# Optimization experiments

Measured on AMD Instinct MI355X. Metric: run time of the kernel, lower is better.

The kernel has to match this reference:

```python
import jax, jax.numpy as jnp
from jax import lax
import numpy as np

N, W, H, C = 32, 64, 64, 256
D_STYLE = 256


def setup_inputs() -> dict:
    key = jax.random.key(0)
    k1, k2, k3, k4 = jax.random.split(key, 4)
    inputs = jax.random.normal(k1, (N, W, H, C), dtype=jnp.float32)
    style_coding = jax.random.normal(k2, (N, D_STYLE), dtype=jnp.float32)
    # he_normal-ish init scaling for the learned weights
    w_dense = jax.random.normal(k3, (D_STYLE, C), dtype=jnp.float32) * np.sqrt(2.0 / D_STYLE)
    w_conv = jax.random.normal(k4, (1, 1, C, C), dtype=jnp.float32) * np.sqrt(2.0 / C)
    return {"inputs": inputs, "style_coding": style_coding, "w_dense": w_dense, "w_conv": w_conv}


def reference(inputs, style_coding, w_dense, w_conv):
    # inputs: [N,W,H,C] (NHWC), style_coding: [N,D_style]
    c = inputs.shape[-1]
    scale = 1.0 / jnp.sqrt(jnp.float32(c))
    # Dense(fout_dim, use_bias=False, activation=LeakyReLU())  (keras default alpha=0.3)
    q = jax.nn.leaky_relu(style_coding @ w_dense, negative_slope=0.3)  # [N,C]
    # channel-wise attention: einsum('nwhc,nwhc->nc') with q broadcast over w,h
    ca_logits = jnp.einsum('nwhc,nc->nc', inputs, q) * scale           # [N,C]
    ca = jax.nn.softmax(ca_logits, axis=-1)[:, None, None, :]          # [N,1,1,C]
    # position-wise attention: einsum('nwhc,nwhc->nwh'), softmax over flattened W*H
    pa_logits = jnp.einsum('nwhc,nc->nwh', inputs, q) * scale          # [N,W,H]
    n, w, h = pa_logits.shape
    pa = jax.nn.softmax(pa_logits.reshape(n, w * h), axis=1).reshape(n, w, h, 1)
    x = inputs * ca * pa                                               # [N,W,H,C]
    # DarknetConv2D_BN_Leaky with no norm kwarg: 1x1 conv (no bias) + LeakyReLU(0.1)
    y = lax.conv_general_dilated(x, w_conv, window_strides=(1, 1), padding='SAME',
                                 dimension_numbers=('NHWC', 'HWIO', 'NHWC'))
    return jax.nn.leaky_relu(y, negative_slope=0.1)
```

## Files before the change

kernel.cpp:

```cpp
#include <hip/hip_runtime.h>
#include <hip/hip_bf16.h>


#define NBATCH 32
#define PIX 4096
#define CH 256
#define SCALE 0.0625f

typedef __attribute__((ext_vector_type(8))) short short8;
typedef __attribute__((ext_vector_type(4))) short short4v;
typedef __attribute__((ext_vector_type(4))) float floatx4;

__device__ __forceinline__ short f2bf(float x) {
    unsigned u = __builtin_bit_cast(unsigned, x);
    u += 0x7fffu + ((u >> 16) & 1u);
    return (short)(u >> 16);
}

__global__ __launch_bounds__(256) void style_kernel(
    const float* __restrict__ style, const float* __restrict__ wd,
    float* __restrict__ q, float* __restrict__ colsum)
{
    __shared__ float s[256];
    const int n = blockIdx.x, t = threadIdx.x;
    s[t] = style[n * 256 + t];
    __syncthreads();
    float acc = 0.f;
#pragma unroll 8
    for (int k = 0; k < 256; ++k) acc += s[k] * wd[k * 256 + t];
    q[n * 256 + t] = acc > 0.f ? acc : 0.3f * acc;
    colsum[n * 256 + t] = 0.f;
}

__global__ __launch_bounds__(256) void reduce_convert_kernel(
    const float* __restrict__ inp, const float* __restrict__ q,
    float* __restrict__ colsum, float* __restrict__ pa_logits,
    short* __restrict__ in_bf)
{
    __shared__ float sm[4][256];
    const int n = blockIdx.y;
    const int chunk = blockIdx.x;
    const int lane = threadIdx.x & 63, w = threadIdx.x >> 6;
    const float4 qv = *(const float4*)&q[n * 256 + lane * 4];
    float4 cs = make_float4(0.f, 0.f, 0.f, 0.f);
    const int pbase = chunk * 128 + w * 32;
    const float* base = inp + ((size_t)n * PIX + pbase) * CH;
    short* bfb = in_bf + ((size_t)n * PIX + pbase) * CH;
    for (int j = 0; j < 32; ++j) {
        float4 v = *(const float4*)&base[(size_t)j * CH + lane * 4];
        short4v s;
        s.x = f2bf(v.x); s.y = f2bf(v.y); s.z = f2bf(v.z); s.w = f2bf(v.w);
        *(short4v*)&bfb[(size_t)j * CH + lane * 4] = s;
        float d = v.x * qv.x + v.y * qv.y + v.z * qv.z + v.w * qv.w;
        cs.x += v.x; cs.y += v.y; cs.z += v.z; cs.w += v.w;
#pragma unroll
        for (int off = 32; off; off >>= 1) d += __shfl_xor(d, off);
        if (lane == 0) pa_logits[n * PIX + pbase + j] = d * SCALE;
    }
    *(float4*)&sm[w][lane * 4] = cs;
    __syncthreads();
    const int t = threadIdx.x;
    float tot = sm[0][t] + sm[1][t] + sm[2][t] + sm[3][t];
    atomicAdd(&colsum[n * 256 + t], tot);
}

__global__ __launch_bounds__(256) void softmax_kernel(
    const float* __restrict__ colsum, const float* __restrict__ q,
    const float* __restrict__ pa_logits,
    float* __restrict__ ca, float* __restrict__ pa)
{
    __shared__ float red[256];
    const int n = blockIdx.x, t = threadIdx.x;

    float lg = colsum[n * 256 + t] * q[n * 256 + t] * SCALE;
    red[t] = lg; __syncthreads();
    for (int s = 128; s > 0; s >>= 1) {
        if (t < s) red[t] = fmaxf(red[t], red[t + s]);
        __syncthreads();
    }
    float m = red[0]; __syncthreads();
    float e = expf(lg - m);
    red[t] = e; __syncthreads();
    for (int s = 128; s > 0; s >>= 1) {
        if (t < s) red[t] += red[t + s];
        __syncthreads();
    }
    ca[n * 256 + t] = e / red[0];
    __syncthreads();

    float lv[16];
    float lmax = -1e30f;
#pragma unroll
    for (int i = 0; i < 16; ++i) {
        lv[i] = pa_logits[n * PIX + t + 256 * i];
        lmax = fmaxf(lmax, lv[i]);
    }
    red[t] = lmax; __syncthreads();
    for (int s = 128; s > 0; s >>= 1) {
        if (t < s) red[t] = fmaxf(red[t], red[t + s]);
        __syncthreads();
    }
    float M = red[0]; __syncthreads();
    float ev[16], lsum = 0.f;
#pragma unroll
    for (int i = 0; i < 16; ++i) { ev[i] = expf(lv[i] - M); lsum += ev[i]; }
    red[t] = lsum; __syncthreads();
    for (int s = 128; s > 0; s >>= 1) {
        if (t < s) red[t] += red[t + s];
        __syncthreads();
    }
    float inv = 1.0f / red[0];
#pragma unroll
    for (int i = 0; i < 16; ++i) pa[n * PIX + t + 256 * i] = ev[i] * inv;
}

__global__ void fold_kernel(const float* __restrict__ wc,
                            const float* __restrict__ ca,
                            short* __restrict__ wn)
{
    __shared__ float tile[32][33];
    const int co0 = blockIdx.x * 32, n = blockIdx.y;
    const int tx = threadIdx.x, ty = threadIdx.y;
    short* wout = wn + (size_t)n * 65536;
    for (int cit = 0; cit < 8; ++cit) {
        const int ci0 = cit * 32;
        if (cit) __syncthreads();
#pragma unroll
        for (int r = 0; r < 4; ++r)
            tile[ty + r * 8][tx] = wc[(ci0 + ty + r * 8) * 256 + co0 + tx];
        __syncthreads();
        const float cav = ca[n * 256 + ci0 + tx];
#pragma unroll
        for (int r = 0; r < 4; ++r)
            wout[(co0 + ty + r * 8) * 256 + ci0 + tx] = f2bf(tile[tx][ty + r * 8] * cav);
    }
}

__global__ __launch_bounds__(256) void conv_mfma(
    const short* __restrict__ in_bf, const float* __restrict__ pa,
    const short* __restrict__ wn, float* __restrict__ out)
{
    __shared__ __attribute__((aligned(16))) short As[128][72];
    __shared__ __attribute__((aligned(16))) short Bs[128][72];

    const int n   = blockIdx.z;
    const int m0  = blockIdx.y * 128;
    const int co0 = blockIdx.x * 128;
    const int tid = threadIdx.x;
    const int lane = tid & 63, wid = tid >> 6;
    const int wm = wid & 1, wn_ = wid >> 1;
    const int l16 = lane & 15, quad = lane >> 4;

    floatx4 acc[4][4] = {};

    const short* Abase = in_bf + ((size_t)(n * PIX + m0)) * CH;
    const short* Bbase = wn + (size_t)n * 65536 + (size_t)co0 * CH;

    const int g = tid & 7, r0 = tid >> 3;

    for (int kb = 0; kb < 4; ++kb) {
        const int k0 = kb * 64;
        if (kb) __syncthreads();
#pragma unroll
        for (int i = 0; i < 4; ++i) {
            const int r = r0 + 32 * i;
            *(uint4*)&As[r][g * 8] = *(const uint4*)&Abase[(size_t)r * CH + k0 + g * 8];
            *(uint4*)&Bs[r][g * 8] = *(const uint4*)&Bbase[(size_t)r * CH + k0 + g * 8];
        }
        __syncthreads();
#pragma unroll
        for (int kk = 0; kk < 64; kk += 32) {
            short8 af[4], bfr[4];
#pragma unroll
            for (int mt = 0; mt < 4; ++mt)
                af[mt] = *(const short8*)&As[wm * 64 + mt * 16 + l16][kk + quad * 8];
#pragma unroll
            for (int nt = 0; nt < 4; ++nt)
                bfr[nt] = *(const short8*)&Bs[wn_ * 64 + nt * 16 + l16][kk + quad * 8];
#pragma unroll
            for (int mt = 0; mt < 4; ++mt)
#pragma unroll
                for (int nt = 0; nt < 4; ++nt)
                    acc[mt][nt] = __builtin_amdgcn_mfma_f32_16x16x32_bf16(
                        af[mt], bfr[nt], acc[mt][nt], 0, 0, 0);
        }
    }

#pragma unroll
    for (int mt = 0; mt < 4; ++mt) {
#pragma unroll
        for (int reg = 0; reg < 4; ++reg) {
            const int pix = m0 + wm * 64 + mt * 16 + quad * 4 + reg;
            const float pav = pa[n * PIX + pix];
            float* orow = out + ((size_t)(n * PIX + pix)) * CH + co0 + wn_ * 64;
#pragma unroll
            for (int nt = 0; nt < 4; ++nt) {
                float z = acc[mt][nt][reg] * pav;
                orow[nt * 16 + l16] = z > 0.f ? z : 0.1f * z;
            }
        }
    }
}

extern "C" void kernel_launch(void* const* d_in, const int* in_sizes, int n_in,
                              void* d_out, int out_size, void* d_ws, size_t ws_size,
                              hipStream_t stream) {
    const float* inputs = (const float*)d_in[0];
    const float* style  = (const float*)d_in[1];
    const float* wdense = (const float*)d_in[2];
    const float* wconv  = (const float*)d_in[3];
    float* out = (float*)d_out;

    char* ws = (char*)d_ws;
    float* q         = (float*)(ws + 0);
    float* colsum    = (float*)(ws + 32768);
    float* ca        = (float*)(ws + 65536);
    float* pa_logits = (float*)(ws + 98304);
    float* pa        = (float*)(ws + 622592);
    short* wn        = (short*)(ws + 1146880);
    short* in_bf     = (short*)(ws + 5341184);

    style_kernel<<<NBATCH, 256, 0, stream>>>(style, wdense, q, colsum);
    reduce_convert_kernel<<<dim3(32, NBATCH), 256, 0, stream>>>(
        inputs, q, colsum, pa_logits, in_bf);
    softmax_kernel<<<NBATCH, 256, 0, stream>>>(colsum, q, pa_logits, ca, pa);
    fold_kernel<<<dim3(8, NBATCH), dim3(32, 8), 0, stream>>>(wconv, ca, wn);
    conv_mfma<<<dim3(2, 32, NBATCH), 256, 0, stream>>>(in_bf, pa, wn, out);
}
```

Measured before the change: 318.0 us.

## Fuse softmaxes into neighbors and load GEMM tiles directly to LDS

Drops the separate position softmax by accumulating exp-sums with atomics during the reduction pass and normalizing in the conv epilogue. It also merges the channel softmax into the weight-fold kernel, removing one launch and the ca/pa round trips. The conv staging switches to global_load_lds direct-to-LDS copies with an unpadded tile, which may add LDS bank conflicts on fragment reads. Skipping max subtraction risks overflow if logits are large.

Measured after the change: 322.9 us. No clear change (+1.5%).

```diff
diff --git a/kernel.cpp b/kernel.cpp
--- a/kernel.cpp
+++ b/kernel.cpp
@@ -11,6 +11,9 @@
 typedef __attribute__((ext_vector_type(4))) short short4v;
 typedef __attribute__((ext_vector_type(4))) float floatx4;
 
+typedef __attribute__((address_space(3))) unsigned lds_u32;
+typedef const __attribute__((address_space(1))) unsigned gbl_u32;
+
 __device__ __forceinline__ short f2bf(float x) {
     unsigned u = __builtin_bit_cast(unsigned, x);
     u += 0x7fffu + ((u >> 16) & 1u);
@@ -19,7 +22,7 @@
 
 __global__ __launch_bounds__(256) void style_kernel(
     const float* __restrict__ style, const float* __restrict__ wd,
-    float* __restrict__ q, float* __restrict__ colsum)
+    float* __restrict__ q, float* __restrict__ colsum, float* __restrict__ Ssum)
 {
     __shared__ float s[256];
     const int n = blockIdx.x, t = threadIdx.x;
@@ -30,12 +33,13 @@
     for (int k = 0; k < 256; ++k) acc += s[k] * wd[k * 256 + t];
     q[n * 256 + t] = acc > 0.f ? acc : 0.3f * acc;
     colsum[n * 256 + t] = 0.f;
+    if (t == 0) Ssum[n] = 0.f;
 }
 
 __global__ __launch_bounds__(256) void reduce_convert_kernel(
     const float* __restrict__ inp, const float* __restrict__ q,
     float* __restrict__ colsum, float* __restrict__ pa_logits,
-    short* __restrict__ in_bf)
+    float* __restrict__ Ssum, short* __restrict__ in_bf)
 {
     __shared__ float sm[4][256];
     const int n = blockIdx.y;
@@ -46,6 +50,7 @@
     const int pbase = chunk * 128 + w * 32;
     const float* base = inp + ((size_t)n * PIX + pbase) * CH;
     short* bfb = in_bf + ((size_t)n * PIX + pbase) * CH;
+    float es = 0.f;
     for (int j = 0; j < 32; ++j) {
         float4 v = *(const float4*)&base[(size_t)j * CH + lane * 4];
         short4v s;
@@ -55,8 +60,13 @@
         cs.x += v.x; cs.y += v.y; cs.z += v.z; cs.w += v.w;
 #pragma unroll
         for (int off = 32; off; off >>= 1) d += __shfl_xor(d, off);
-        if (lane == 0) pa_logits[n * PIX + pbase + j] = d * SCALE;
-    }
+        if (lane == 0) {
+            const float lg = d * SCALE;
+            pa_logits[n * PIX + pbase + j] = lg;
+            es += __expf(lg);
+        }
+    }
+    if (lane == 0) atomicAdd(&Ssum[n], es);
     *(float4*)&sm[w][lane * 4] = cs;
     __syncthreads();
     const int t = threadIdx.x;
@@ -64,13 +74,14 @@
     atomicAdd(&colsum[n * 256 + t], tot);
 }
 
-__global__ __launch_bounds__(256) void softmax_kernel(
+__global__ __launch_bounds__(256) void ca_fold_kernel(
     const float* __restrict__ colsum, const float* __restrict__ q,
-    const float* __restrict__ pa_logits,
-    float* __restrict__ ca, float* __restrict__ pa)
+    const float* __restrict__ wc, short* __restrict__ wn)
 {
     __shared__ float red[256];
-    const int n = blockIdx.x, t = threadIdx.x;
+    __shared__ float cas[256];
+    __shared__ float tile[32][33];
+    const int n = blockIdx.y, t = threadIdx.x;
 
     float lg = colsum[n * 256 + t] * q[n * 256 + t] * SCALE;
     red[t] = lg; __syncthreads();
@@ -79,48 +90,17 @@
         __syncthreads();
     }
     float m = red[0]; __syncthreads();
-    float e = expf(lg - m);
+    float e = __expf(lg - m);
     red[t] = e; __syncthreads();
     for (int s = 128; s > 0; s >>= 1) {
         if (t < s) red[t] += red[t + s];
         __syncthreads();
     }
-    ca[n * 256 + t] = e / red[0];
+    cas[t] = e / red[0];
     __syncthreads();
 
-    float lv[16];
-    float lmax = -1e30f;
-#pragma unroll
-    for (int i = 0; i < 16; ++i) {
-        lv[i] = pa_logits[n * PIX + t + 256 * i];
-        lmax = fmaxf(lmax, lv[i]);
-    }
-    red[t] = lmax; __syncthreads();
-    for (int s = 128; s > 0; s >>= 1) {
-        if (t < s) red[t] = fmaxf(red[t], red[t + s]);
-        __syncthreads();
-    }
-    float M = red[0]; __syncthreads();
-    float ev[16], lsum = 0.f;
-#pragma unroll
-    for (int i = 0; i < 16; ++i) { ev[i] = expf(lv[i] - M); lsum += ev[i]; }
-    red[t] = lsum; __syncthreads();
-    for (int s = 128; s > 0; s >>= 1) {
-        if (t < s) red[t] += red[t + s];
-        __syncthreads();
-    }
-    float inv = 1.0f / red[0];
-#pragma unroll
-    for (int i = 0; i < 16; ++i) pa[n * PIX + t + 256 * i] = ev[i] * inv;
-}
-
-__global__ void fold_kernel(const float* __restrict__ wc,
-                            const float* __restrict__ ca,
-                            short* __restrict__ wn)
-{
-    __shared__ float tile[32][33];
-    const int co0 = blockIdx.x * 32, n = blockIdx.y;
-    const int tx = threadIdx.x, ty = threadIdx.y;
+    const int co0 = blockIdx.x * 32;
+    const int tx = t & 31, ty = t >> 5;
     short* wout = wn + (size_t)n * 65536;
     for (int cit = 0; cit < 8; ++cit) {
         const int ci0 = cit * 32;
@@ -129,7 +109,7 @@
         for (int r = 0; r < 4; ++r)
             tile[ty + r * 8][tx] = wc[(ci0 + ty + r * 8) * 256 + co0 + tx];
         __syncthreads();
-        const float cav = ca[n * 256 + ci0 + tx];
+        const float cav = cas[ci0 + tx];
 #pragma unroll
         for (int r = 0; r < 4; ++r)
             wout[(co0 + ty + r * 8) * 256 + ci0 + tx] = f2bf(tile[tx][ty + r * 8] * cav);
@@ -137,11 +117,12 @@
 }
 
 __global__ __launch_bounds__(256) void conv_mfma(
-    const short* __restrict__ in_bf, const float* __restrict__ pa,
-    const short* __restrict__ wn, float* __restrict__ out)
-{
-    __shared__ __attribute__((aligned(16))) short As[128][72];
-    __shared__ __attribute__((aligned(16))) short Bs[128][72];
+    const short* __restrict__ in_bf, const float* __restrict__ pa_logits,
+    const float* __restrict__ Ssum, const short* __restrict__ wn,
+    float* __restrict__ out)
+{
+    __shared__ __attribute__((aligned(16))) short As[128 * 64];
+    __shared__ __attribute__((aligned(16))) short Bs[128 * 64];
 
     const int n   = blockIdx.z;
     const int m0  = blockIdx.y * 128;
@@ -150,22 +131,25 @@
     const int lane = tid & 63, wid = tid >> 6;
     const int wm = wid & 1, wn_ = wid >> 1;
     const int l16 = lane & 15, quad = lane >> 4;
+    const int lr = lane >> 3, lc = lane & 7;
 
     floatx4 acc[4][4] = {};
 
-    const short* Abase = in_bf + ((size_t)(n * PIX + m0)) * CH;
-    const short* Bbase = wn + (size_t)n * 65536 + (size_t)co0 * CH;
-
-    const int g = tid & 7, r0 = tid >> 3;
+    const short* Ab = in_bf + ((size_t)(n * PIX + m0)) * CH;
+    const short* Bb = wn + (size_t)n * 65536 + (size_t)co0 * CH;
 
     for (int kb = 0; kb < 4; ++kb) {
         const int k0 = kb * 64;
         if (kb) __syncthreads();
 #pragma unroll
-        for (int i = 0; i < 4; ++i) {
-            const int r = r0 + 32 * i;
-            *(uint4*)&As[r][g * 8] = *(const uint4*)&Abase[(size_t)r * CH + k0 + g * 8];
-            *(uint4*)&Bs[r][g * 8] = *(const uint4*)&Bbase[(size_t)r * CH + k0 + g * 8];
+        for (int c = 0; c < 4; ++c) {
+            const int r = 32 * wid + 8 * c + lr;
+            __builtin_amdgcn_global_load_lds(
+                (gbl_u32*)(Ab + (size_t)r * CH + k0 + lc * 8),
+                (lds_u32*)(&As[(32 * wid + 8 * c) * 64]), 16, 0, 0);
+            __builtin_amdgcn_global_load_lds(
+                (gbl_u32*)(Bb + (size_t)r * CH + k0 + lc * 8),
+                (lds_u32*)(&Bs[(32 * wid + 8 * c) * 64]), 16, 0, 0);
         }
         __syncthreads();
 #pragma unroll
@@ -173,10 +157,10 @@
             short8 af[4], bfr[4];
 #pragma unroll
             for (int mt = 0; mt < 4; ++mt)
-                af[mt] = *(const short8*)&As[wm * 64 + mt * 16 + l16][kk + quad * 8];
+                af[mt] = *(const short8*)&As[(wm * 64 + mt * 16 + l16) * 64 + kk + quad * 8];
 #pragma unroll
             for (int nt = 0; nt < 4; ++nt)
-                bfr[nt] = *(const short8*)&Bs[wn_ * 64 + nt * 16 + l16][kk + quad * 8];
+                bfr[nt] = *(const short8*)&Bs[(wn_ * 64 + nt * 16 + l16) * 64 + kk + quad * 8];
 #pragma unroll
             for (int mt = 0; mt < 4; ++mt)
 #pragma unroll
@@ -186,12 +170,13 @@
         }
     }
 
+    const float invS = 1.0f / Ssum[n];
 #pragma unroll
     for (int mt = 0; mt < 4; ++mt) {
 #pragma unroll
         for (int reg = 0; reg < 4; ++reg) {
             const int pix = m0 + wm * 64 + mt * 16 + quad * 4 + reg;
-            const float pav = pa[n * PIX + pix];
+            const float pav = __expf(pa_logits[n * PIX + pix]) * invS;
             float* orow = out + ((size_t)(n * PIX + pix)) * CH + co0 + wn_ * 64;
 #pragma unroll
             for (int nt = 0; nt < 4; ++nt) {
@@ -214,16 +199,14 @@
     char* ws = (char*)d_ws;
     float* q         = (float*)(ws + 0);
     float* colsum    = (float*)(ws + 32768);
-    float* ca        = (float*)(ws + 65536);
-    float* pa_logits = (float*)(ws + 98304);
-    float* pa        = (float*)(ws + 622592);
-    short* wn        = (short*)(ws + 1146880);
-    short* in_bf     = (short*)(ws + 5341184);
-
-    style_kernel<<<NBATCH, 256, 0, stream>>>(style, wdense, q, colsum);
+    float* Ssum      = (float*)(ws + 65536);
+    float* pa_logits = (float*)(ws + 69632);
+    short* wn        = (short*)(ws + 593920);
+    short* in_bf     = (short*)(ws + 4788224);
+
+    style_kernel<<<NBATCH, 256, 0, stream>>>(style, wdense, q, colsum, Ssum);
     reduce_convert_kernel<<<dim3(32, NBATCH), 256, 0, stream>>>(
-        inputs, q, colsum, pa_logits, in_bf);
-    softmax_kernel<<<NBATCH, 256, 0, stream>>>(colsum, q, pa_logits, ca, pa);
-    fold_kernel<<<dim3(8, NBATCH), dim3(32, 8), 0, stream>>>(wconv, ca, wn);
-    conv_mfma<<<dim3(2, 32, NBATCH), 256, 0, stream>>>(in_bf, pa, wn, out);
-}
+        inputs, q, colsum, pa_logits, Ssum, in_bf);
+    ca_fold_kernel<<<dim3(8, NBATCH), 256, 0, stream>>>(colsum, q, wconv, wn);
+    conv_mfma<<<dim3(2, 32, NBATCH), 256, 0, stream>>>(in_bf, pa_logits, Ssum, wn, out);
+}
```
